# Kernel tuning notes

Hardware: AMD Instinct MI355X
Metric: run time of the kernel (lower is better)

Reference implementation:

```python
import jax, jax.numpy as jnp
import numpy as np

B, S, H = 2, 2048, 2560
N_HEADS, N_KV, HEAD_DIM = 8, 4, 256
QUERY_PRE_ATTN_SCALAR = 256.0
SOFTCAP = 50.0
SLIDING_WINDOW = 1024
EPS = 1e-6
MASK_MIN = -1e9


def setup_inputs() -> dict:
    key = jax.random.key(0)
    ks = jax.random.split(key, 8)
    hidden_states = jax.random.normal(ks[0], (B, S, H), jnp.float32)
    # RoPE tables (real Gemma3 rotary embedding)
    inv_freq = 1.0 / (10000.0 ** (np.arange(0, HEAD_DIM, 2, dtype=np.float32) / HEAD_DIM))
    pos = np.arange(S, dtype=np.float32)
    freqs = np.outer(pos, inv_freq)                     # [S, D/2]
    emb = np.concatenate([freqs, freqs], axis=-1)       # [S, D]
    cos = jnp.broadcast_to(jnp.asarray(np.cos(emb)), (B, S, HEAD_DIM))
    sin = jnp.broadcast_to(jnp.asarray(np.sin(emb)), (B, S, HEAD_DIM))
    # causal + sliding-window additive mask [B,1,S,S]
    i = np.arange(S)[:, None]
    j = np.arange(S)[None, :]
    allowed = (j <= i) & (j > i - SLIDING_WINDOW)
    mask = np.where(allowed, 0.0, MASK_MIN).astype(np.float32)
    attention_mask = jnp.broadcast_to(jnp.asarray(mask)[None, None], (B, 1, S, S))
    sc = 0.02
    wq = jax.random.normal(ks[1], (N_HEADS * HEAD_DIM, H), jnp.float32) * sc
    wk = jax.random.normal(ks[2], (N_KV * HEAD_DIM, H), jnp.float32) * sc
    wv = jax.random.normal(ks[3], (N_KV * HEAD_DIM, H), jnp.float32) * sc
    wo = jax.random.normal(ks[4], (H, N_HEADS * HEAD_DIM), jnp.float32) * sc
    q_norm_w = jnp.zeros((HEAD_DIM,), jnp.float32)  # Gemma norm uses (1 + w)
    k_norm_w = jnp.zeros((HEAD_DIM,), jnp.float32)
    return {"hidden_states": hidden_states, "cos": cos, "sin": sin,
            "attention_mask": attention_mask, "wq": wq, "wk": wk, "wv": wv,
            "wo": wo, "q_norm_w": q_norm_w, "k_norm_w": k_norm_w}


def _gemma_rms_norm(x, w):
    # Gemma3 RMSNorm over head_dim in float32, scale = (1 + w)
    xf = x.astype(jnp.float32)
    n = xf * jax.lax.rsqrt(jnp.mean(xf * xf, axis=-1, keepdims=True) + EPS)
    return (n * (1.0 + w.astype(jnp.float32))).astype(x.dtype)


def _rotate_half(x):
    x1, x2 = jnp.split(x, 2, axis=-1)
    return jnp.concatenate([-x2, x1], axis=-1)


def _apply_rope(q, k, cos, sin):
    cos = cos[:, None]  # [B,1,S,D] -> broadcast over heads
    sin = sin[:, None]
    return q * cos + _rotate_half(q) * sin, k * cos + _rotate_half(k) * sin


def reference(hidden_states, cos, sin, attention_mask, wq, wk, wv, wo, q_norm_w, k_norm_w):
    Bq, Sq, _ = hidden_states.shape
    n_rep = N_HEADS // N_KV
    # projections (quantizers are identity here) -> [B, heads, S, D]
    q = (hidden_states @ wq.T).reshape(Bq, Sq, N_HEADS, HEAD_DIM).transpose(0, 2, 1, 3)
    k = (hidden_states @ wk.T).reshape(Bq, Sq, N_KV, HEAD_DIM).transpose(0, 2, 1, 3)
    v = (hidden_states @ wv.T).reshape(Bq, Sq, N_KV, HEAD_DIM).transpose(0, 2, 1, 3)
    q = _gemma_rms_norm(q, q_norm_w)
    k = _gemma_rms_norm(k, k_norm_w)
    q, k = _apply_rope(q, k, cos, sin)
    # GQA repeat kv
    k = jnp.repeat(k, n_rep, axis=1)
    v = jnp.repeat(v, n_rep, axis=1)
    scaling = QUERY_PRE_ATTN_SCALAR ** -0.5
    scores = jnp.einsum('bhqd,bhkd->bhqk', q, k) * scaling
    scores = jnp.tanh(scores / SOFTCAP) * SOFTCAP
    scores = scores + attention_mask
    attn = jax.nn.softmax(scores.astype(jnp.float32), axis=-1).astype(q.dtype)
    out = jnp.einsum('bhqk,bhkd->bhqd', attn, v)
    out = out.transpose(0, 2, 1, 3).reshape(Bq, Sq, N_HEADS * HEAD_DIM)
    attn_output = out @ wo.T
    return attn_output
```

## Files before the change

### kernel.cpp

```cpp
#include <hip/hip_runtime.h>
#include <hip/hip_bf16.h>

#define S_LEN 2048
#define HDIM  256
#define NHq   8
#define NKV   4

typedef __attribute__((ext_vector_type(8))) __bf16 bf16x8;
typedef __attribute__((ext_vector_type(4))) float  f32x4;

#define MFMA16x16(a,b,c) __builtin_amdgcn_mfma_f32_16x16x32_bf16((a),(b),(c),0,0,0)

__device__ __forceinline__ unsigned short f2b(float f) {
  return __builtin_bit_cast(unsigned short, (__bf16)f);
}
__device__ __forceinline__ float b2f(unsigned short u) {
  return (float)__builtin_bit_cast(__bf16, u);
}
__device__ __forceinline__ void gl_lds16(const void* g, void* l) {
  __builtin_amdgcn_global_load_lds(
      (const __attribute__((address_space(1))) unsigned int*)g,
      (__attribute__((address_space(3))) unsigned int*)l, 16, 0, 0);
}

__global__ __launch_bounds__(256) void cast_f32_bf16(
    const float* __restrict__ in, unsigned short* __restrict__ out, int n4) {
  int idx = blockIdx.x * blockDim.x + threadIdx.x;
  int stride = gridDim.x * blockDim.x;
  for (int i = idx; i < n4; i += stride) {
    float4 v = ((const float4*)in)[i];
    ushort4 o;
    o.x = f2b(v.x); o.y = f2b(v.y); o.z = f2b(v.z); o.w = f2b(v.w);
    ((ushort4*)out)[i] = o;
  }
}

template<int MODE>
__global__ __launch_bounds__(256) void gemm_bt(
    const unsigned short* __restrict__ A,
    const unsigned short* __restrict__ Bw,
    int K,
    unsigned short* __restrict__ q_out,
    unsigned short* __restrict__ k_out,
    unsigned short* __restrict__ vT_out,
    float* __restrict__ f_out, int Nf) {
  __shared__ unsigned short As[128 * 32];
  __shared__ unsigned short Bs[128 * 32];
  const int t = threadIdx.x;
  const int m0 = blockIdx.x * 128;
  const int n0 = blockIdx.y * 128;
  const int w = t >> 6, l = t & 63;
  const int wr = (w >> 1) * 64, wc = (w & 1) * 64;
  const int lr = l & 15, g = l >> 4;

  f32x4 acc[4][4] = {};

  const int Lrow = t >> 2;
  const int Lkb  = ((t & 3) * 16) ^ ((Lrow & 3) << 4);
  const char* Ab  = (const char*)A  + ((size_t)(m0 + Lrow) * K) * 2 + Lkb;
  const char* Ab2 = Ab + (size_t)64 * K * 2;
  const char* Bb  = (const char*)Bw + ((size_t)(n0 + Lrow) * K) * 2 + Lkb;
  const char* Bb2 = Bb + (size_t)64 * K * 2;
  char* ldsA = (char*)As + t * 16;
  char* ldsB = (char*)Bs + t * 16;

  for (int k0 = 0; k0 < K; k0 += 32) {
    gl_lds16(Ab  + (size_t)k0 * 2, ldsA);
    gl_lds16(Ab2 + (size_t)k0 * 2, ldsA + 4096);
    gl_lds16(Bb  + (size_t)k0 * 2, ldsB);
    gl_lds16(Bb2 + (size_t)k0 * 2, ldsB + 4096);
    __syncthreads();
    bf16x8 af[4], bfr[4];
#pragma unroll
    for (int fm = 0; fm < 4; fm++) {
      int byteo = (wr + fm * 16 + lr) * 64 + g * 16;
      int sb = byteo ^ (((byteo >> 6) & 3) << 4);
      af[fm] = *(const bf16x8*)((const char*)As + sb);
    }
#pragma unroll
    for (int fn = 0; fn < 4; fn++) {
      int byteo = (wc + fn * 16 + lr) * 64 + g * 16;
      int sb = byteo ^ (((byteo >> 6) & 3) << 4);
      bfr[fn] = *(const bf16x8*)((const char*)Bs + sb);
    }
#pragma unroll
    for (int fm = 0; fm < 4; fm++)
#pragma unroll
      for (int fn = 0; fn < 4; fn++)
        acc[fm][fn] = MFMA16x16(af[fm], bfr[fn], acc[fm][fn]);
    __syncthreads();
  }

  const int mb = m0 + wr + g * 4;
  const int nb = n0 + wc + lr;
  if (MODE == 1) {
#pragma unroll
    for (int fm = 0; fm < 4; fm++)
#pragma unroll
      for (int fn = 0; fn < 4; fn++)
#pragma unroll
        for (int r = 0; r < 4; r++) {
          int m = mb + fm * 16 + r;
          int n = nb + fn * 16;
          f_out[(size_t)m * Nf + n] = acc[fm][fn][r];
        }
  } else {
#pragma unroll
    for (int fm = 0; fm < 4; fm++)
#pragma unroll
      for (int fn = 0; fn < 4; fn++)
#pragma unroll
        for (int r = 0; r < 4; r++) {
          int m = mb + fm * 16 + r;
          int n = nb + fn * 16;
          int b = m >> 11, s = m & 2047;
          unsigned short val = f2b(acc[fm][fn][r]);
          if (n0 < 2048) {
            int h = n >> 8, d = n & 255;
            q_out[(((size_t)(b * 8 + h) * 2048) + s) * 256 + d] = val;
          } else if (n0 < 3072) {
            int kv = (n - 2048) >> 8, d = n & 255;
            k_out[(((size_t)(b * 4 + kv) * 2048) + s) * 256 + d] = val;
          } else {
            int kv = (n - 3072) >> 8, d = n & 255;
            vT_out[(((size_t)(b * 4 + kv) * 256) + d) * 2048 + s] = val;
          }
        }
  }
}

__global__ __launch_bounds__(256) void norm_rope(
    unsigned short* __restrict__ Qb, unsigned short* __restrict__ Kb,
    const float* __restrict__ cosb, const float* __restrict__ sinb,
    const float* __restrict__ qw, const float* __restrict__ kw) {
  const int row = blockIdx.x * 4 + (threadIdx.x >> 6);
  const int l = threadIdx.x & 63;
  unsigned short* base;
  int b, s;
  const float* wp;
  if (row < 32768) {
    base = Qb + (size_t)row * 256;
    b = row >> 14; s = row & 2047; wp = qw;
  } else {
    int r = row - 32768;
    base = Kb + (size_t)r * 256;
    b = r >> 13; s = r & 2047; wp = kw;
  }
  const int d = l * 4;
  ushort4 xu = *(const ushort4*)(base + d);
  float x0 = b2f(xu.x), x1 = b2f(xu.y), x2 = b2f(xu.z), x3 = b2f(xu.w);
  float ss = x0 * x0 + x1 * x1 + x2 * x2 + x3 * x3;
#pragma unroll
  for (int mk = 1; mk < 64; mk <<= 1) ss += __shfl_xor(ss, mk, 64);
  const float rinv = rsqrtf(ss * (1.0f / 256.0f) + 1e-6f);
  const float4 wv = *(const float4*)(wp + d);
  float n0 = x0 * rinv * (1.f + wv.x);
  float n1 = x1 * rinv * (1.f + wv.y);
  float n2 = x2 * rinv * (1.f + wv.z);
  float n3 = x3 * rinv * (1.f + wv.w);
  float p0 = __shfl_xor(n0, 32, 64);
  float p1 = __shfl_xor(n1, 32, 64);
  float p2 = __shfl_xor(n2, 32, 64);
  float p3 = __shfl_xor(n3, 32, 64);
  const float sgn = (l < 32) ? -1.f : 1.f;
  const size_t cofs = ((size_t)(b * 2048 + s)) * 256 + d;
  const float4 cv = *(const float4*)(cosb + cofs);
  const float4 sv = *(const float4*)(sinb + cofs);
  xu.x = f2b(n0 * cv.x + sgn * p0 * sv.x);
  xu.y = f2b(n1 * cv.y + sgn * p1 * sv.y);
  xu.z = f2b(n2 * cv.z + sgn * p2 * sv.z);
  xu.w = f2b(n3 * cv.w + sgn * p3 * sv.w);
  *(ushort4*)(base + d) = xu;
}

__global__ __launch_bounds__(256) void attn_fwd(
    const unsigned short* __restrict__ Qb,
    const unsigned short* __restrict__ Kb,
    const unsigned short* __restrict__ VTb,
    unsigned short* __restrict__ Ob) {
  __shared__ __align__(16) unsigned char smem[65536];
  unsigned short* Ks = (unsigned short*)smem;
  const char* Vsc = (const char*)(smem + 32768);
  const int t = threadIdx.x, w = t >> 6, l = t & 63;
  const int qt = blockIdx.x, h = blockIdx.y, b = blockIdx.z;
  const int kvh = h >> 1;
  const int i0 = qt * 64, iw = i0 + w * 16;
  const int lr = l & 15, g = l >> 4, g4 = g * 4;
  char* PsB = (char*)(smem + w * 2048);

  bf16x8 qf[8];
  {
    const unsigned short* qrow = Qb + (((size_t)(b * 8 + h) * 2048) + iw + lr) * 256;
#pragma unroll
    for (int ks = 0; ks < 8; ks++) qf[ks] = *(const bf16x8*)(qrow + ks * 32 + g * 8);
  }
  f32x4 accO[16] = {};
  float mrow[4] = {-3e38f, -3e38f, -3e38f, -3e38f};
  float lrow[4] = {0.f, 0.f, 0.f, 0.f};

  const int jt0 = (qt >= 16) ? (qt - 16) : 0;
  const unsigned short* Kt  = Kb  + ((size_t)(b * 4 + kvh) * 2048) * 256;
  const unsigned short* VTt = VTb + ((size_t)(b * 4 + kvh) * 256) * 2048;

  for (int jt = jt0; jt <= qt; jt++) {
    const char* Kg = (const char*)(Kt + (size_t)jt * 64 * 256);
#pragma unroll
    for (int qq = 0; qq < 8; qq++) {
      int L = t * 16 + qq * 4096;
      int Lsw = L ^ (((L >> 9) & 7) << 4);
      gl_lds16(Kg + Lsw, (char*)Ks + L);
    }
#pragma unroll
    for (int qq = 0; qq < 8; qq++) {
      int L = t * 16 + qq * 4096;
      int Ls = L ^ (((L >> 7) & 7) << 4);
      int dd = Ls >> 7, kb = Ls & 127;
      const char* src = (const char*)(VTt + (size_t)dd * 2048 + (size_t)jt * 64) + kb;
      gl_lds16(src, (char*)smem + 32768 + L);
    }
    __syncthreads();

    f32x4 sc[4];
#pragma unroll
    for (int fn = 0; fn < 4; fn++) {
      f32x4 a = {0.f, 0.f, 0.f, 0.f};
      int j = fn * 16 + lr;
#pragma unroll
      for (int ks = 0; ks < 8; ks++) {
        int byteo = j * 512 + ks * 64 + g * 16;
        int sb = byteo ^ (((byteo >> 9) & 7) << 4);
        bf16x8 kf = *(const bf16x8*)((const char*)Ks + sb);
        a = MFMA16x16(qf[ks], kf, a);
      }
      sc[fn] = a;
    }

    const int jbase = jt * 64;
    float sv4[4][4];
#pragma unroll
    for (int fn = 0; fn < 4; fn++) {
      int j = jbase + fn * 16 + lr;
#pragma unroll
      for (int r = 0; r < 4; r++) {
        float s = sc[fn][r];
        float xx = s * 0.00125f;
        float e2 = __expf(xx + xx);
        s = 50.f * (e2 - 1.f) / (e2 + 1.f);
        int i = iw + g4 + r;
        bool ok = (j <= i) && (j > i - 1024);
        sv4[r][fn] = ok ? s : -1e9f;
      }
    }
    float pw[4][4];
#pragma unroll
    for (int r = 0; r < 4; r++) {
      float pm = fmaxf(fmaxf(sv4[r][0], sv4[r][1]), fmaxf(sv4[r][2], sv4[r][3]));
      pm = fmaxf(pm, __shfl_xor(pm, 1, 64));
      pm = fmaxf(pm, __shfl_xor(pm, 2, 64));
      pm = fmaxf(pm, __shfl_xor(pm, 4, 64));
      pm = fmaxf(pm, __shfl_xor(pm, 8, 64));
      float mnew = fmaxf(mrow[r], pm);
      float alpha = __expf(mrow[r] - mnew);
      mrow[r] = mnew;
      float ps = 0.f;
#pragma unroll
      for (int fn = 0; fn < 4; fn++) {
        float p = __expf(sv4[r][fn] - mnew);
        pw[r][fn] = p; ps += p;
      }
      ps += __shfl_xor(ps, 1, 64);
      ps += __shfl_xor(ps, 2, 64);
      ps += __shfl_xor(ps, 4, 64);
      ps += __shfl_xor(ps, 8, 64);
      lrow[r] = lrow[r] * alpha + ps;
#pragma unroll
      for (int fd = 0; fd < 16; fd++) accO[fd][r] *= alpha;
    }

    __syncthreads();
#pragma unroll
    for (int r = 0; r < 4; r++)
#pragma unroll
      for (int fn = 0; fn < 4; fn++) {
        int byteo = (g4 + r) * 128 + (fn * 16 + lr) * 2;
        int sb = byteo ^ (((byteo >> 7) & 7) << 4);
        *(unsigned short*)(PsB + sb) = f2b(pw[r][fn]);
      }
    __syncthreads();

    bf16x8 pf[2];
#pragma unroll
    for (int k2 = 0; k2 < 2; k2++) {
      int byteo = lr * 128 + k2 * 64 + g * 16;
      int sb = byteo ^ (((byteo >> 7) & 7) << 4);
      pf[k2] = *(const bf16x8*)(PsB + sb);
    }
#pragma unroll
    for (int fd = 0; fd < 16; fd++) {
#pragma unroll
      for (int k2 = 0; k2 < 2; k2++) {
        int vb = (fd * 16 + lr) * 128 + k2 * 64 + g * 16;
        int sb = vb ^ (((vb >> 7) & 7) << 4);
        bf16x8 vf = *(const bf16x8*)(Vsc + sb);
        accO[fd] = MFMA16x16(pf[k2], vf, accO[fd]);
      }
    }
    __syncthreads();
  }

  float inv[4];
#pragma unroll
  for (int r = 0; r < 4; r++) inv[r] = 1.f / lrow[r];
#pragma unroll
  for (int fd = 0; fd < 16; fd++)
#pragma unroll
    for (int r = 0; r < 4; r++) {
      int i = iw + g4 + r;
      int dd = fd * 16 + lr;
      Ob[((size_t)(b * 2048 + i)) * 2048 + h * 256 + dd] = f2b(accO[fd][r] * inv[r]);
    }
}

extern "C" void kernel_launch(void* const* d_in, const int* in_sizes, int n_in,
                              void* d_out, int out_size, void* d_ws, size_t ws_size,
                              hipStream_t stream) {
  (void)in_sizes; (void)n_in; (void)out_size; (void)ws_size;
  const float* hs   = (const float*)d_in[0];
  const float* cosb = (const float*)d_in[1];
  const float* sinb = (const float*)d_in[2];
  const float* wq   = (const float*)d_in[4];
  const float* wk   = (const float*)d_in[5];
  const float* wv   = (const float*)d_in[6];
  const float* wo   = (const float*)d_in[7];
  const float* qnw  = (const float*)d_in[8];
  const float* knw  = (const float*)d_in[9];

  char* ws = (char*)d_ws;
  unsigned short* Xbf  = (unsigned short*)(ws);
  unsigned short* Wqkv = (unsigned short*)(ws + 20971520);
  unsigned short* Wob  = (unsigned short*)(ws + 41943040);
  unsigned short* Qb   = (unsigned short*)(ws + 52428800);
  unsigned short* Kb   = (unsigned short*)(ws + 69206016);
  unsigned short* VT   = (unsigned short*)(ws + 77594624);
  unsigned short* AO   = (unsigned short*)(ws + 85983232);

  cast_f32_bf16<<<2048, 256, 0, stream>>>(hs, Xbf, 10485760 / 4);
  cast_f32_bf16<<<1024, 256, 0, stream>>>(wq, Wqkv, 5242880 / 4);
  cast_f32_bf16<<<512,  256, 0, stream>>>(wk, Wqkv + 5242880, 2621440 / 4);
  cast_f32_bf16<<<512,  256, 0, stream>>>(wv, Wqkv + 7864320, 2621440 / 4);
  cast_f32_bf16<<<1024, 256, 0, stream>>>(wo, Wob, 5242880 / 4);

  dim3 g0(32, 32);
  gemm_bt<0><<<g0, 256, 0, stream>>>(Xbf, Wqkv, 2560, Qb, Kb, VT, nullptr, 0);

  norm_rope<<<12288, 256, 0, stream>>>(Qb, Kb, cosb, sinb, qnw, knw);

  dim3 ga(32, 8, 2);
  attn_fwd<<<ga, 256, 0, stream>>>(Qb, Kb, VT, AO);

  dim3 g1(32, 20);
  gemm_bt<1><<<g1, 256, 0, stream>>>(AO, Wob, 2048, nullptr, nullptr, nullptr,
                                     (float*)d_out, 2560);
}
```

Baseline: 533.3 us.

## Double-buffer GEMM LDS staging with BK=64, larger QKV tiles, MFMA priority hints

Replaces the single-buffered GEMM with a templated two-phase kernel that prefetches the next K-tile of 64 into a second LDS slot while computing on the current one, halving barrier count per K. The QKV projection uses 256x256 tiles with 512 threads and 8 waves, which raises data reuse per block. The attention kernel wraps its MFMA loops in s_setprio to favor matrix issue. The larger tiles use much more LDS (128 KB for the QKV GEMM) and grid 16x16=256 blocks, which may limit occupancy.

```diff
diff --git a/kernel.cpp b/kernel.cpp
--- a/kernel.cpp
+++ b/kernel.cpp
@@ -35,8 +35,8 @@
   }
 }
 
-template<int MODE>
-__global__ __launch_bounds__(256) void gemm_bt(
+template<int MODE, int BM, int BN, int WM, int WN, int THREADS>
+__global__ __launch_bounds__(THREADS, 2) void gemm2ph(
     const unsigned short* __restrict__ A,
     const unsigned short* __restrict__ Bw,
     int K,
@@ -44,60 +44,89 @@
     unsigned short* __restrict__ k_out,
     unsigned short* __restrict__ vT_out,
     float* __restrict__ f_out, int Nf) {
-  __shared__ unsigned short As[128 * 32];
-  __shared__ unsigned short Bs[128 * 32];
+  constexpr int ASLOT = BM * 64;
+  constexpr int BSLOT = BN * 64;
+  __shared__ unsigned short As[2 * ASLOT];
+  __shared__ unsigned short Bs[2 * BSLOT];
   const int t = threadIdx.x;
-  const int m0 = blockIdx.x * 128;
-  const int n0 = blockIdx.y * 128;
+  const int m0 = blockIdx.x * BM;
+  const int n0 = blockIdx.y * BN;
   const int w = t >> 6, l = t & 63;
-  const int wr = (w >> 1) * 64, wc = (w & 1) * 64;
+  const int wm = w / WN, wn = w % WN;
+  constexpr int WROWS = BM / WM;
+  constexpr int WCOLS = BN / WN;
+  constexpr int MF = WROWS / 16;
+  constexpr int NF = WCOLS / 16;
+  const int wrow = wm * WROWS, wcol = wn * WCOLS;
   const int lr = l & 15, g = l >> 4;
 
-  f32x4 acc[4][4] = {};
-
-  const int Lrow = t >> 2;
-  const int Lkb  = ((t & 3) * 16) ^ ((Lrow & 3) << 4);
-  const char* Ab  = (const char*)A  + ((size_t)(m0 + Lrow) * K) * 2 + Lkb;
-  const char* Ab2 = Ab + (size_t)64 * K * 2;
-  const char* Bb  = (const char*)Bw + ((size_t)(n0 + Lrow) * K) * 2 + Lkb;
-  const char* Bb2 = Bb + (size_t)64 * K * 2;
-  char* ldsA = (char*)As + t * 16;
-  char* ldsB = (char*)Bs + t * 16;
-
-  for (int k0 = 0; k0 < K; k0 += 32) {
-    gl_lds16(Ab  + (size_t)k0 * 2, ldsA);
-    gl_lds16(Ab2 + (size_t)k0 * 2, ldsA + 4096);
-    gl_lds16(Bb  + (size_t)k0 * 2, ldsB);
-    gl_lds16(Bb2 + (size_t)k0 * 2, ldsB + 4096);
-    __syncthreads();
-    bf16x8 af[4], bfr[4];
-#pragma unroll
-    for (int fm = 0; fm < 4; fm++) {
-      int byteo = (wr + fm * 16 + lr) * 64 + g * 16;
-      int sb = byteo ^ (((byteo >> 6) & 3) << 4);
-      af[fm] = *(const bf16x8*)((const char*)As + sb);
-    }
-#pragma unroll
-    for (int fn = 0; fn < 4; fn++) {
-      int byteo = (wc + fn * 16 + lr) * 64 + g * 16;
-      int sb = byteo ^ (((byteo >> 6) & 3) << 4);
-      bfr[fn] = *(const bf16x8*)((const char*)Bs + sb);
-    }
-#pragma unroll
-    for (int fm = 0; fm < 4; fm++)
-#pragma unroll
-      for (int fn = 0; fn < 4; fn++)
-        acc[fm][fn] = MFMA16x16(af[fm], bfr[fn], acc[fm][fn]);
-    __syncthreads();
-  }
-
-  const int mb = m0 + wr + g * 4;
-  const int nb = n0 + wc + lr;
+  f32x4 acc[MF][NF] = {};
+
+  constexpr int CHA = BM * 128 / (THREADS * 16);
+  constexpr int CHB = BN * 128 / (THREADS * 16);
+  const int r0 = t >> 3;
+  const int cb = (t & 7) * 16;
+  const int cbs = cb ^ ((r0 & 7) << 4);
+  const char* Asrc = (const char*)A  + ((size_t)(m0 + r0) * K) * 2 + cbs;
+  const char* Bsrc = (const char*)Bw + ((size_t)(n0 + r0) * K) * 2 + cbs;
+  const size_t rstep = (size_t)(THREADS / 8) * K * 2;
+
+  auto STAGE = [&](int slot, int k0) {
+    char* la = (char*)(As + slot * ASLOT) + t * 16;
+    char* lb = (char*)(Bs + slot * BSLOT) + t * 16;
+    const char* ga = Asrc + (size_t)k0 * 2;
+    const char* gb = Bsrc + (size_t)k0 * 2;
+#pragma unroll
+    for (int q = 0; q < CHA; q++) gl_lds16(ga + q * rstep, la + q * THREADS * 16);
+#pragma unroll
+    for (int q = 0; q < CHB; q++) gl_lds16(gb + q * rstep, lb + q * THREADS * 16);
+  };
+
+  auto COMPUTE = [&](int slot) {
+    const char* ab = (const char*)(As + slot * ASLOT);
+    const char* bb = (const char*)(Bs + slot * BSLOT);
+#pragma unroll
+    for (int ks = 0; ks < 2; ks++) {
+      bf16x8 af[MF], bfr[NF];
+#pragma unroll
+      for (int fm = 0; fm < MF; fm++) {
+        int row = wrow + fm * 16 + lr;
+        int byo = row * 128 + ((ks * 64 + g * 16) ^ ((row & 7) << 4));
+        af[fm] = *(const bf16x8*)(ab + byo);
+      }
+#pragma unroll
+      for (int fn = 0; fn < NF; fn++) {
+        int row = wcol + fn * 16 + lr;
+        int byo = row * 128 + ((ks * 64 + g * 16) ^ ((row & 7) << 4));
+        bfr[fn] = *(const bf16x8*)(bb + byo);
+      }
+#pragma unroll
+      for (int fm = 0; fm < MF; fm++)
+#pragma unroll
+        for (int fn = 0; fn < NF; fn++)
+          acc[fm][fn] = MFMA16x16(af[fm], bfr[fn], acc[fm][fn]);
+    }
+  };
+
+  STAGE(0, 0);
+  __syncthreads();
+  int cur = 0;
+  const int NT = K >> 6;
+  for (int tt = 0; tt < NT - 1; tt++) {
+    STAGE(cur ^ 1, (tt + 1) * 64);
+    COMPUTE(cur);
+    __syncthreads();
+    cur ^= 1;
+  }
+  COMPUTE(cur);
+
+  const int mb = m0 + wrow + g * 4;
+  const int nb = n0 + wcol + lr;
   if (MODE == 1) {
 #pragma unroll
-    for (int fm = 0; fm < 4; fm++)
-#pragma unroll
-      for (int fn = 0; fn < 4; fn++)
+    for (int fm = 0; fm < MF; fm++)
+#pragma unroll
+      for (int fn = 0; fn < NF; fn++)
 #pragma unroll
         for (int r = 0; r < 4; r++) {
           int m = mb + fm * 16 + r;
@@ -106,9 +135,9 @@
         }
   } else {
 #pragma unroll
-    for (int fm = 0; fm < 4; fm++)
-#pragma unroll
-      for (int fn = 0; fn < 4; fn++)
+    for (int fm = 0; fm < MF; fm++)
+#pragma unroll
+      for (int fn = 0; fn < NF; fn++)
 #pragma unroll
         for (int r = 0; r < 4; r++) {
           int m = mb + fm * 16 + r;
@@ -221,6 +250,7 @@
     __syncthreads();
 
     f32x4 sc[4];
+    __builtin_amdgcn_s_setprio(1);
 #pragma unroll
     for (int fn = 0; fn < 4; fn++) {
       f32x4 a = {0.f, 0.f, 0.f, 0.f};
@@ -234,6 +264,7 @@
       }
       sc[fn] = a;
     }
+    __builtin_amdgcn_s_setprio(0);
 
     const int jbase = jt * 64;
     float sv4[4][4];
@@ -295,6 +326,7 @@
       int sb = byteo ^ (((byteo >> 7) & 7) << 4);
       pf[k2] = *(const bf16x8*)(PsB + sb);
     }
+    __builtin_amdgcn_s_setprio(1);
 #pragma unroll
     for (int fd = 0; fd < 16; fd++) {
 #pragma unroll
@@ -305,6 +337,7 @@
         accO[fd] = MFMA16x16(pf[k2], vf, accO[fd]);
       }
     }
+    __builtin_amdgcn_s_setprio(0);
     __syncthreads();
   }
 
@@ -350,8 +383,9 @@
   cast_f32_bf16<<<512,  256, 0, stream>>>(wv, Wqkv + 7864320, 2621440 / 4);
   cast_f32_bf16<<<1024, 256, 0, stream>>>(wo, Wob, 5242880 / 4);
 
-  dim3 g0(32, 32);
-  gemm_bt<0><<<g0, 256, 0, stream>>>(Xbf, Wqkv, 2560, Qb, Kb, VT, nullptr, 0);
+  dim3 g0(16, 16);
+  gemm2ph<0, 256, 256, 2, 4, 512><<<g0, 512, 0, stream>>>(
+      Xbf, Wqkv, 2560, Qb, Kb, VT, nullptr, 0);
 
   norm_rope<<<12288, 256, 0, stream>>>(Qb, Kb, cosb, sinb, qnw, knw);
 
@@ -359,6 +393,6 @@
   attn_fwd<<<ga, 256, 0, stream>>>(Qb, Kb, VT, AO);
 
   dim3 g1(32, 20);
-  gemm_bt<1><<<g1, 256, 0, stream>>>(AO, Wob, 2048, nullptr, nullptr, nullptr,
-                                     (float*)d_out, 2560);
-}
+  gemm2ph<1, 128, 128, 2, 2, 256><<<g1, 256, 0, stream>>>(
+      AO, Wob, 2048, nullptr, nullptr, nullptr, (float*)d_out, 2560);
+}
```

Result: no change. 542.0 us (+1.6%).
